# Performance work log

Hardware: AMD Instinct MI355X
Metric: run time of the kernel (lower is better)

Reference implementation:

```python
import jax, jax.numpy as jnp
import numpy as np

N, E = 50000, 800000
IN, HID, H1, H2, OUT = 128, 64, 4, 6, 121
NEG_SLOPE = 0.2


def setup_inputs() -> dict:
    key = jax.random.key(0)
    ks = jax.random.split(key, 16)
    s = 0.1  # weight init scale
    return {
        "x": jax.random.normal(ks[0], (N, IN), jnp.float32),
        "src": jax.random.randint(ks[1], (E,), 0, N),
        "dst": jax.random.randint(ks[2], (E,), 0, N),
        # conv1: in=IN, heads=H1, out=HID, concat
        "W1": jax.random.normal(ks[3], (IN, H1 * HID), jnp.float32) * s,
        "a1_src": jax.random.normal(ks[4], (H1, HID), jnp.float32) * s,
        "a1_dst": jax.random.normal(ks[5], (H1, HID), jnp.float32) * s,
        "b1": jnp.zeros((H1 * HID,), jnp.float32),
        # conv2: in=H1*HID, heads=H1, out=HID, concat, residual
        "W2": jax.random.normal(ks[6], (H1 * HID, H1 * HID), jnp.float32) * s,
        "a2_src": jax.random.normal(ks[7], (H1, HID), jnp.float32) * s,
        "a2_dst": jax.random.normal(ks[8], (H1, HID), jnp.float32) * s,
        "b2": jnp.zeros((H1 * HID,), jnp.float32),
        "Wres2": jax.random.normal(ks[9], (H1 * HID, H1 * HID), jnp.float32) * s,
        # conv3: in=H1*HID, heads=H2, out=OUT, mean (concat=False)
        "W3": jax.random.normal(ks[10], (H1 * HID, H2 * OUT), jnp.float32) * s,
        "a3_src": jax.random.normal(ks[11], (H2, OUT), jnp.float32) * s,
        "a3_dst": jax.random.normal(ks[12], (H2, OUT), jnp.float32) * s,
        "b3": jnp.zeros((OUT,), jnp.float32),
    }


def _segment_softmax(e, seg, n):
    # e: [E, H], softmax over edges sharing the same destination node
    m = jax.ops.segment_max(e, seg, num_segments=n)
    ex = jnp.exp(e - m[seg])
    s = jax.ops.segment_sum(ex, seg, num_segments=n)
    return ex / (s[seg] + 1e-16)


def _gat_conv(x, src, dst, W, a_src, a_dst, b, heads, ch, concat, Wres=None):
    n = x.shape[0]
    h = (x @ W).reshape(n, heads, ch)                       # [N, H, C]
    al_s = jnp.sum(h * a_src, axis=-1)                      # [N, H]
    al_d = jnp.sum(h * a_dst, axis=-1)                      # [N, H]
    e = jax.nn.leaky_relu(al_s[src] + al_d[dst], NEG_SLOPE)  # [E, H]
    alpha = _segment_softmax(e, dst, n)                     # [E, H]
    msg = h[src] * alpha[..., None]                         # [E, H, C]
    out = jax.ops.segment_sum(msg, dst, num_segments=n)     # [N, H, C]
    out = out.reshape(n, heads * ch) if concat else out.mean(axis=1)
    if Wres is not None:
        out = out + x @ Wres
    return out + b


def reference(x, src, dst, W1, a1_src, a1_dst, b1, W2, a2_src, a2_dst, b2,
              Wres2, W3, a3_src, a3_dst, b3):
    n = x.shape[0]
    # PyG GATConv default: add self-loops
    loop = jnp.arange(n, dtype=src.dtype)
    s = jnp.concatenate([src, loop])
    d = jnp.concatenate([dst, loop])
    h = jax.nn.elu(_gat_conv(x, s, d, W1, a1_src, a1_dst, b1, H1, HID, True))
    h = jax.nn.elu(_gat_conv(h, s, d, W2, a2_src, a2_dst, b2, H1, HID, True, Wres=Wres2))
    h = _gat_conv(h, s, d, W3, a3_src, a3_dst, b3, H2, OUT, False)
    return jax.nn.sigmoid(h)
```

## Files before the change

### kernel.cpp

```cpp
#include <hip/hip_runtime.h>
#include <hip/hip_bf16.h>


#define NODES 50000
#define EDGES 800000
#define MPAD  50048
#define C0    25088
#define C1    24912

typedef unsigned short u16;
typedef __attribute__((ext_vector_type(8))) short bf16x8;
typedef __attribute__((ext_vector_type(4))) float f32x4;

__device__ __forceinline__ float bf16f(u16 r) {
    return __uint_as_float(((unsigned)r) << 16);
}
__device__ __forceinline__ u16 f2b(float v) {
    __hip_bfloat16 b = __float2bfloat16(v);
    return *(u16*)&b;
}
__device__ __forceinline__ float blo(unsigned d) { return __uint_as_float(d << 16); }
__device__ __forceinline__ float bhi(unsigned d) { return __uint_as_float(d & 0xffff0000u); }


__global__ void fill_ones_kernel(int* __restrict__ deg, int n) {
    int i = blockIdx.x * blockDim.x + threadIdx.x;
    if (i < n) deg[i] = 1;
}

__global__ void hist_kernel(const int* __restrict__ dst, int* __restrict__ deg, int E) {
    int e = blockIdx.x * blockDim.x + threadIdx.x;
    if (e < E) atomicAdd(&deg[dst[e]], 1);
}

__global__ void deg_bsum_kernel(const int* __restrict__ deg, int* __restrict__ bsum, int n) {
    int tid = threadIdx.x, lane = tid & 63, wid = tid >> 6;
    int i = blockIdx.x * 256 + tid;
    int v = (i < n) ? deg[i] : 0;
    #pragma unroll
    for (int ofs = 32; ofs > 0; ofs >>= 1) v += __shfl_down(v, ofs);
    __shared__ int sp[4];
    if (lane == 0) sp[wid] = v;
    __syncthreads();
    if (tid == 0) bsum[blockIdx.x] = sp[0] + sp[1] + sp[2] + sp[3];
}

__global__ void bsum_scan_kernel(int* __restrict__ bsum, int* __restrict__ row_ptr,
                                 int nb, int n) {
    int tid = threadIdx.x, lane = tid & 63, wid = tid >> 6;
    int v = (tid < nb) ? bsum[tid] : 0;
    int incl = v;
    #pragma unroll
    for (int ofs = 1; ofs < 64; ofs <<= 1) {
        int t = __shfl_up(incl, ofs);
        if (lane >= ofs) incl += t;
    }
    __shared__ int sp[4];
    if (lane == 63) sp[wid] = incl;
    __syncthreads();
    int add = 0;
    for (int k = 0; k < wid; k++) add += sp[k];
    int excl = incl - v + add;
    if (tid < nb) bsum[tid] = excl;
    if (tid == nb - 1) row_ptr[n] = excl + v;
}

__global__ void deg_scan_kernel(const int* __restrict__ deg, const int* __restrict__ bofs,
                                int* __restrict__ row_ptr, int* __restrict__ cursor, int n) {
    int tid = threadIdx.x, lane = tid & 63, wid = tid >> 6;
    int i = blockIdx.x * 256 + tid;
    int v = (i < n) ? deg[i] : 0;
    int incl = v;
    #pragma unroll
    for (int ofs = 1; ofs < 64; ofs <<= 1) {
        int t = __shfl_up(incl, ofs);
        if (lane >= ofs) incl += t;
    }
    __shared__ int sp[4];
    if (lane == 63) sp[wid] = incl;
    __syncthreads();
    int add = bofs[blockIdx.x];
    for (int k = 0; k < wid; k++) add += sp[k];
    int excl = incl - v + add;
    if (i < n) { row_ptr[i] = excl; cursor[i] = excl; }
}

__global__ void scatter_kernel(const int* __restrict__ src, const int* __restrict__ dst,
                               int E, int n, int* __restrict__ cursor, int* __restrict__ csr_src) {
    int e = blockIdx.x * blockDim.x + threadIdx.x;
    if (e < E) {
        int d = dst[e];
        int p = atomicAdd(&cursor[d], 1);
        csr_src[p] = src[e];
    } else if (e < E + n) {
        int i = e - E;
        int p = atomicAdd(&cursor[i], 1);
        csr_src[p] = i;
    }
}


__global__ void prep_weights(
    const float* __restrict__ W1, const float* __restrict__ W2,
    const float* __restrict__ Wres2, const float* __restrict__ W3,
    const float* __restrict__ a1s, const float* __restrict__ a1d,
    const float* __restrict__ a2s, const float* __restrict__ a2d,
    const float* __restrict__ a3s, const float* __restrict__ a3d,
    u16* __restrict__ WT1, u16* __restrict__ WT2, u16* __restrict__ W3sT,
    float* __restrict__ q1t, float* __restrict__ q2t, float* __restrict__ cm) {
    int idx = blockIdx.x * 256 + threadIdx.x;
    if (idx < 32768) {
        int n = idx >> 7, k = idx & 127;
        WT1[idx] = f2b(W1[(size_t)k * 256 + n]);
    } else if ((idx -= 32768) < 131072) {
        int n = idx >> 8, k = idx & 255;
        float v = (n < 256) ? W2[(size_t)k * 256 + n] : Wres2[(size_t)k * 256 + (n - 256)];
        WT2[idx] = f2b(v);
    } else if ((idx -= 131072) < 196608) {
        int n = idx / 1536, q = idx % 1536;
        int h = q >> 8, k = q & 255;
        W3sT[idx] = f2b((n < 121) ? W3[(size_t)k * 726 + h * 121 + n] : 0.f);
    } else if ((idx -= 196608) < 1024) {
        int h = idx >> 7, k = idx & 127;
        int hh = h & 3;
        const float* a = (h < 4) ? a1s : a1d;
        float v = 0.f;
        for (int c = 0; c < 64; c++) v += W1[(size_t)k * 256 + hh * 64 + c] * a[hh * 64 + c];
        q1t[idx] = v;
    } else if ((idx -= 1024) < 2048) {
        int h = idx >> 8, k = idx & 255;
        int hh = h & 3;
        const float* a = (h < 4) ? a2s : a2d;
        float v = 0.f;
        for (int c = 0; c < 64; c++) v += W2[(size_t)k * 256 + hh * 64 + c] * a[hh * 64 + c];
        q2t[idx] = v;
    } else if ((idx -= 2048) < 3072) {
        int o = idx >> 8, k = idx & 255;
        int h = (o < 6) ? o : o - 6;
        const float* a = (o < 6) ? a3s : a3d;
        float v = 0.f;
        for (int c = 0; c < 121; c++) v += W3[(size_t)k * 726 + h * 121 + c] * a[h * 121 + c];
        cm[idx] = v;
    }
}
#define PREP_TOTAL (32768 + 131072 + 196608 + 1024 + 2048 + 3072)


__global__ __launch_bounds__(256) void convx_al1(
    const float* __restrict__ x, const float* __restrict__ q1t,
    u16* __restrict__ A2a, float* __restrict__ alA, int n) {
    int wid = threadIdx.x >> 6, lane = threadIdx.x & 63;
    int i = blockIdx.x * 4 + wid;
    if (i >= n) return;
    float2 xv = *(const float2*)(x + (size_t)i * 128 + lane * 2);
    ushort2 o;
    o.x = f2b(xv.x); o.y = f2b(xv.y);
    *(ushort2*)(A2a + (size_t)i * 128 + lane * 2) = o;
    float p[8];
    #pragma unroll
    for (int h = 0; h < 8; h++) {
        float2 q = *(const float2*)(q1t + h * 128 + lane * 2);
        p[h] = xv.x * q.x + xv.y * q.y;
    }
    #pragma unroll
    for (int ofs = 1; ofs <= 32; ofs <<= 1) {
        #pragma unroll
        for (int h = 0; h < 8; h++) p[h] += __shfl_xor(p[h], ofs);
    }
    if (lane == 0) {
        *(float4*)(alA + (size_t)i * 8)     = make_float4(p[0], p[1], p[2], p[3]);
        *(float4*)(alA + (size_t)i * 8 + 4) = make_float4(p[4], p[5], p[6], p[7]);
    }
}


__global__ __launch_bounds__(256) void gemm_mfma_kernel(
    const u16* __restrict__ A, const u16* __restrict__ B,
    u16* __restrict__ Cb, u16* __restrict__ Cb2,
    int M, int K2, int ldc, int split, int NT, int nrt) {
    __shared__ __align__(16) u16 smem[2][128][40];
    #define As smem[0]
    #define Bs smem[1]
    int b = blockIdx.x;
    int xcd = b & 7, q = b >> 3;
    int ct = q % NT, rb = q / NT;
    int rt = rb * 8 + xcd;
    if (rt >= nrt) return;
    int bm = rt * 128, bn = ct * 128;

    int tid = threadIdx.x;
    int lane = tid & 63;
    int wv = tid >> 6;
    int quad = lane >> 4, lm = lane & 15;
    int wm = (wv & 1) * 64, wn = (wv >> 1) * 64;

    int lrow0 = tid >> 2, lseg0 = (tid & 3) * 8;
    int lrow1 = (tid + 256) >> 2, lseg1 = ((tid + 256) & 3) * 8;
    const u16* Ap0 = A + (size_t)(bm + lrow0) * K2 + lseg0;
    const u16* Ap1 = A + (size_t)(bm + lrow1) * K2 + lseg1;
    const u16* Bp0 = B + (size_t)(bn + lrow0) * K2 + lseg0;
    const u16* Bp1 = B + (size_t)(bn + lrow1) * K2 + lseg1;

    f32x4 zero = {0.f, 0.f, 0.f, 0.f};
    f32x4 acc[4][4];
    #pragma unroll
    for (int i = 0; i < 4; i++)
        #pragma unroll
        for (int j = 0; j < 4; j++) acc[i][j] = zero;

    uint4 pa0 = *(const uint4*)(Ap0), pa1 = *(const uint4*)(Ap1);
    uint4 pb0 = *(const uint4*)(Bp0), pb1 = *(const uint4*)(Bp1);

    for (int k0 = 0; k0 < K2; k0 += 32) {
        *(uint4*)&As[lrow0][lseg0] = pa0;
        *(uint4*)&As[lrow1][lseg1] = pa1;
        *(uint4*)&Bs[lrow0][lseg0] = pb0;
        *(uint4*)&Bs[lrow1][lseg1] = pb1;
        __syncthreads();
        bool more = (k0 + 32) < K2;
        if (more) {
            pa0 = *(const uint4*)(Ap0 + k0 + 32);
            pa1 = *(const uint4*)(Ap1 + k0 + 32);
            pb0 = *(const uint4*)(Bp0 + k0 + 32);
            pb1 = *(const uint4*)(Bp1 + k0 + 32);
        }
        bf16x8 af[4], bfr[4];
        #pragma unroll
        for (int i = 0; i < 4; i++) af[i] = *(const bf16x8*)&As[wm + i * 16 + lm][quad * 8];
        #pragma unroll
        for (int j = 0; j < 4; j++) bfr[j] = *(const bf16x8*)&Bs[wn + j * 16 + lm][quad * 8];
        #pragma unroll
        for (int i = 0; i < 4; i++)
            #pragma unroll
            for (int j = 0; j < 4; j++)
                acc[i][j] = __builtin_amdgcn_mfma_f32_16x16x32_bf16(af[i], bfr[j], acc[i][j], 0, 0, 0);
        __syncthreads();
    }

    u16* Cp = (bn < split) ? (Cb + bn) : (Cb2 + (bn - split));
    u16 (*St)[136] = (u16(*)[136])&smem[0][0][0];
    #pragma unroll
    for (int halfrow = 0; halfrow < 2; ++halfrow) {
        __syncthreads();
        if ((wv & 1) == halfrow) {
            #pragma unroll
            for (int i = 0; i < 4; i++) {
                int lr = i * 16 + quad * 4;
                #pragma unroll
                for (int j = 0; j < 4; j++) {
                    int lc = wn + j * 16 + lm;
                    #pragma unroll
                    for (int r = 0; r < 4; r++)
                        St[lr + r][lc] = f2b(acc[i][j][r]);
                }
            }
        }
        __syncthreads();
        #pragma unroll
        for (int it = 0; it < 4; ++it) {
            int idx = tid + it * 256;
            int row = idx >> 4, seg = idx & 15;
            int grow = bm + halfrow * 64 + row;
            if (grow < M)
                *(uint4*)(Cp + (size_t)grow * ldc + seg * 8) = *(const uint4*)&St[row][seg * 8];
        }
    }
    #undef As
    #undef Bs
}


__global__ __launch_bounds__(256) void gemm_skinny64(
    const u16* __restrict__ A, const u16* __restrict__ B,
    float* __restrict__ C, const float* __restrict__ bias, int count) {
    __shared__ __align__(16) u16 As[64][40];
    __shared__ __align__(16) u16 Bs[128][40];
    int tid = threadIdx.x, lane = tid & 63, wv = tid >> 6;
    int quad = lane >> 4, lm = lane & 15;
    int bm = blockIdx.x * 64;
    int mrow = (wv >> 1) * 32, ncol = (wv & 1) * 64;
    int ar = bm + (tid >> 2);
    if (ar >= count) ar = count - 1;
    const u16* Ap = A + (size_t)ar * 1536 + (tid & 3) * 8;
    int brow0 = tid >> 2, bseg0 = (tid & 3) * 8;
    int brow1 = (tid + 256) >> 2, bseg1 = ((tid + 256) & 3) * 8;
    const u16* Bp0 = B + (size_t)brow0 * 1536 + bseg0;
    const u16* Bp1 = B + (size_t)brow1 * 1536 + bseg1;

    f32x4 zero = {0.f, 0.f, 0.f, 0.f};
    f32x4 acc[2][4];
    #pragma unroll
    for (int i = 0; i < 2; i++)
        #pragma unroll
        for (int j = 0; j < 4; j++) acc[i][j] = zero;

    uint4 pa = *(const uint4*)(Ap);
    uint4 pb0 = *(const uint4*)(Bp0);
    uint4 pb1 = *(const uint4*)(Bp1);

    for (int k0 = 0; k0 < 1536; k0 += 32) {
        *(uint4*)&As[tid >> 2][(tid & 3) * 8] = pa;
        *(uint4*)&Bs[brow0][bseg0] = pb0;
        *(uint4*)&Bs[brow1][bseg1] = pb1;
        __syncthreads();
        bool more = (k0 + 32) < 1536;
        if (more) {
            pa  = *(const uint4*)(Ap + k0 + 32);
            pb0 = *(const uint4*)(Bp0 + k0 + 32);
            pb1 = *(const uint4*)(Bp1 + k0 + 32);
        }
        bf16x8 af[2], bfr[4];
        #pragma unroll
        for (int i = 0; i < 2; i++) af[i] = *(const bf16x8*)&As[mrow + i * 16 + lm][quad * 8];
        #pragma unroll
        for (int j = 0; j < 4; j++) bfr[j] = *(const bf16x8*)&Bs[ncol + j * 16 + lm][quad * 8];
        #pragma unroll
        for (int i = 0; i < 2; i++)
            #pragma unroll
            for (int j = 0; j < 4; j++)
                acc[i][j] = __builtin_amdgcn_mfma_f32_16x16x32_bf16(af[i], bfr[j], acc[i][j], 0, 0, 0);
        __syncthreads();
    }

    #pragma unroll
    for (int i = 0; i < 2; i++) {
        #pragma unroll
        for (int j = 0; j < 4; j++) {
            int col = ncol + j * 16 + lm;
            if (col >= 121) continue;
            int row_base = bm + mrow + i * 16 + quad * 4;
            #pragma unroll
            for (int r = 0; r < 4; r++) {
                int row = row_base + r;
                if (row >= count) continue;
                float v = acc[i][j][r] + bias[col];
                v = 1.f / (1.f + __expf(-v));
                C[(size_t)row * 121 + col] = v;
            }
        }
    }
}


#define ACC8(wt, dv) \
    acc[0] = fmaf(wt, blo(dv.x), acc[0]); acc[1] = fmaf(wt, bhi(dv.x), acc[1]); \
    acc[2] = fmaf(wt, blo(dv.y), acc[2]); acc[3] = fmaf(wt, bhi(dv.y), acc[3]); \
    acc[4] = fmaf(wt, blo(dv.z), acc[4]); acc[5] = fmaf(wt, bhi(dv.z), acc[5]); \
    acc[6] = fmaf(wt, blo(dv.w), acc[6]); acc[7] = fmaf(wt, bhi(dv.w), acc[7]);

template <int NH>
__global__ __launch_bounds__(256) void agg4_fused(
    const u16* __restrict__ f, const float* __restrict__ al8,
    const int* __restrict__ row_ptr, const int* __restrict__ csr_src,
    const float* __restrict__ bias, const u16* __restrict__ resb,
    u16* __restrict__ outb, const float* __restrict__ qpost,
    float* __restrict__ alout, int n) {
    constexpr int NH2 = NH / 2;
    int wid = threadIdx.x >> 6, lane = threadIdx.x & 63;
    int i = blockIdx.x * 4 + wid;
    if (i >= n) return;
    int beg = row_ptr[i], end = row_ptr[i + 1];
    int h_st = lane >> 4;
    int el = lane & 15;
    int half = lane >> 5;
    int c8 = (lane & 31) * 8;
    int wsel = (lane & 24) << 1;
    float ald_st = al8[(size_t)i * 8 + 4 + h_st];
    float acc[8] = {};
    float S = 0.f;
    for (int base = beg; base < end; base += 16) {
        int cnt = min(16, end - base);
        int idxv = csr_src[base + min(el, cnt - 1)];
        float av = al8[(size_t)idxv * 8 + h_st] + ald_st;
        av = av > 0.f ? av : 0.2f * av;
        float ex = __expf(fminf(av, 60.f));
        int e = 0;
        for (; e + 8 <= cnt; e += 8) {
            int s0 = __shfl(idxv, e + half);
            int s1 = __shfl(idxv, e + 2 + half);
            int s2 = __shfl(idxv, e + 4 + half);
            int s3 = __shfl(idxv, e + 6 + half);
            uint4 d0 = *(const uint4*)(f + (size_t)s0 * 256 + c8);
            uint4 d1 = *(const uint4*)(f + (size_t)s1 * 256 + c8);
            uint4 d2 = *(const uint4*)(f + (size_t)s2 * 256 + c8);
            uint4 d3 = *(const uint4*)(f + (size_t)s3 * 256 + c8);
            float w0 = __shfl(ex, wsel | (e + half));
            float w1 = __shfl(ex, wsel | (e + 2 + half));
            float w2 = __shfl(ex, wsel | (e + 4 + half));
            float w3 = __shfl(ex, wsel | (e + 6 + half));
            S += (w0 + w1) + (w2 + w3);
            ACC8(w0, d0);
            ACC8(w1, d1);
            ACC8(w2, d2);
            ACC8(w3, d3);
        }
        for (; e + 4 <= cnt; e += 4) {
            int s0 = __shfl(idxv, e + half);
            int s1 = __shfl(idxv, e + 2 + half);
            uint4 d0 = *(const uint4*)(f + (size_t)s0 * 256 + c8);
            uint4 d1 = *(const uint4*)(f + (size_t)s1 * 256 + c8);
            float w0 = __shfl(ex, wsel | (e + half));
            float w1 = __shfl(ex, wsel | (e + 2 + half));
            S += w0 + w1;
            ACC8(w0, d0);
            ACC8(w1, d1);
        }
        for (; e < cnt; e += 2) {
            int ei = e + half;
            int eu = ei < cnt ? ei : e;
            int s = __shfl(idxv, eu);
            float w = __shfl(ex, wsel | eu);
            if (ei >= cnt) w = 0.f;
            S += w;
            uint4 d = *(const uint4*)(f + (size_t)s * 256 + c8);
            ACC8(w, d);
        }
    }
    #pragma unroll
    for (int k = 0; k < 8; k++) acc[k] += __shfl_xor(acc[k], 32);
    S += __shfl_xor(S, 32);
    float inv = 1.f / (S + 1e-16f);
    float4 b0 = *(const float4*)(bias + c8);
    float4 b1 = *(const float4*)(bias + c8 + 4);
    float v[8];
    v[0] = acc[0] * inv + b0.x; v[1] = acc[1] * inv + b0.y;
    v[2] = acc[2] * inv + b0.z; v[3] = acc[3] * inv + b0.w;
    v[4] = acc[4] * inv + b1.x; v[5] = acc[5] * inv + b1.y;
    v[6] = acc[6] * inv + b1.z; v[7] = acc[7] * inv + b1.w;
    if (resb) {
        uint4 r = *(const uint4*)(resb + (size_t)i * 256 + c8);
        v[0] += blo(r.x); v[1] += bhi(r.x); v[2] += blo(r.y); v[3] += bhi(r.y);
        v[4] += blo(r.z); v[5] += bhi(r.z); v[6] += blo(r.w); v[7] += bhi(r.w);
    }
    #pragma unroll
    for (int k = 0; k < 8; k++) v[k] = v[k] > 0.f ? v[k] : (__expf(v[k]) - 1.f);
    uint4 o;
    o.x = (unsigned)f2b(v[0]) | ((unsigned)f2b(v[1]) << 16);
    o.y = (unsigned)f2b(v[2]) | ((unsigned)f2b(v[3]) << 16);
    o.z = (unsigned)f2b(v[4]) | ((unsigned)f2b(v[5]) << 16);
    o.w = (unsigned)f2b(v[6]) | ((unsigned)f2b(v[7]) << 16);
    if (half == 0)
        *(uint4*)(outb + (size_t)i * 256 + c8) = o;
    if (NH > 0) {
        float rv[8];
        rv[0] = blo(o.x); rv[1] = bhi(o.x); rv[2] = blo(o.y); rv[3] = bhi(o.y);
        rv[4] = blo(o.z); rv[5] = bhi(o.z); rv[6] = blo(o.w); rv[7] = bhi(o.w);
        int hbase = half * NH2;
        float p[NH2 > 0 ? NH2 : 1];
        #pragma unroll
        for (int h = 0; h < NH2; h++) {
            const float* qp = qpost + (size_t)(hbase + h) * 256 + c8;
            float4 qa = *(const float4*)(qp);
            float4 qb = *(const float4*)(qp + 4);
            p[h] = rv[0] * qa.x + rv[1] * qa.y + rv[2] * qa.z + rv[3] * qa.w
                 + rv[4] * qb.x + rv[5] * qb.y + rv[6] * qb.z + rv[7] * qb.w;
        }
        #pragma unroll
        for (int ofs = 1; ofs <= 16; ofs <<= 1) {
            #pragma unroll
            for (int h = 0; h < NH2; h++) p[h] += __shfl_xor(p[h], ofs);
        }
        if ((lane & 31) == 0) {
            float* ap = alout + (size_t)i * NH + hbase;
            if (NH2 == 4) {
                *(float4*)ap = make_float4(p[0], p[1], p[2], p[3]);
            } else if (NH2 == 6) {
                if (half == 0) {
                    *(float4*)ap = make_float4(p[0], p[1], p[2], p[3]);
                    *(float2*)(ap + 4) = make_float2(p[4], p[5]);
                } else {
                    *(float2*)ap = make_float2(p[0], p[1]);
                    *(float4*)(ap + 2) = make_float4(p[2], p[3], p[4], p[5]);
                }
            } else {
                #pragma unroll
                for (int h = 0; h < NH2; h++) ap[h] = p[h];
            }
        }
    }
}


__global__ __launch_bounds__(256) void aggS_fused(
    const u16* __restrict__ x, const float* __restrict__ al3,
    const int* __restrict__ row_ptr, const int* __restrict__ csr_src,
    u16* __restrict__ S, int node0, int count) {
    __shared__ int s_i[4][16];
    __shared__ float s_w[4][96];
    __shared__ float s_sum[4][6];
    int wid = threadIdx.x >> 6, lane = threadIdx.x & 63;
    int li = blockIdx.x * 4 + wid;
    if (li >= count) return;
    int i = node0 + li;
    int beg = row_ptr[i], end = row_ptr[i + 1];
    int c4 = lane * 4;
    int e16 = lane & 15;
    int hA = lane >> 4;
    int hB = 4 + (lane >> 4);
    float aldA = al3[(size_t)i * 12 + 6 + hA];
    float aldB = (lane < 32) ? al3[(size_t)i * 12 + 6 + hB] : 0.f;
    float acc[6][4] = {};
    if (lane < 6) s_sum[wid][lane] = 0.f;
    for (int base = beg; base < end; base += 16) {
        int cnt = min(16, end - base);
        int idxe = csr_src[base + min(e16, cnt - 1)];
        if (lane < 16) s_i[wid][lane] = idxe;
        float vA = al3[(size_t)idxe * 12 + hA] + aldA;
        vA = vA > 0.f ? vA : 0.2f * vA;
        float exA = __expf(fminf(vA, 60.f));
        if (e16 < cnt) s_w[wid][e16 * 6 + hA] = exA;
        float exB = 0.f;
        if (lane < 32) {
            float vB = al3[(size_t)idxe * 12 + hB] + aldB;
            vB = vB > 0.f ? vB : 0.2f * vB;
            exB = __expf(fminf(vB, 60.f));
            if (e16 < cnt) s_w[wid][e16 * 6 + hB] = exB;
        }
        float sA = (e16 < cnt) ? exA : 0.f;
        sA += __shfl_xor(sA, 1); sA += __shfl_xor(sA, 2);
        sA += __shfl_xor(sA, 4); sA += __shfl_xor(sA, 8);
        float sB = (lane < 32 && e16 < cnt) ? exB : 0.f;
        sB += __shfl_xor(sB, 1); sB += __shfl_xor(sB, 2);
        sB += __shfl_xor(sB, 4); sB += __shfl_xor(sB, 8);
        if (e16 == 0) {
            s_sum[wid][hA] += sA;
            if (lane < 32) s_sum[wid][hB] += sB;
        }
        int e = 0;
        for (; e + 4 <= cnt; e += 4) {
            int s0 = s_i[wid][e],     s1 = s_i[wid][e + 1];
            int s2 = s_i[wid][e + 2], s3 = s_i[wid][e + 3];
            uint2 d0 = *(const uint2*)(x + (size_t)s0 * 256 + c4);
            uint2 d1 = *(const uint2*)(x + (size_t)s1 * 256 + c4);
            uint2 d2 = *(const uint2*)(x + (size_t)s2 * 256 + c4);
            uint2 d3 = *(const uint2*)(x + (size_t)s3 * 256 + c4);
            float f00 = blo(d0.x), f01 = bhi(d0.x), f02 = blo(d0.y), f03 = bhi(d0.y);
            float f10 = blo(d1.x), f11 = bhi(d1.x), f12 = blo(d1.y), f13 = bhi(d1.y);
            float f20 = blo(d2.x), f21 = bhi(d2.x), f22 = blo(d2.y), f23 = bhi(d2.y);
            float f30 = blo(d3.x), f31 = bhi(d3.x), f32 = blo(d3.y), f33 = bhi(d3.y);
            #pragma unroll
            for (int hh = 0; hh < 6; hh++) {
                float w0 = s_w[wid][e * 6 + hh];
                float w1 = s_w[wid][(e + 1) * 6 + hh];
                float w2 = s_w[wid][(e + 2) * 6 + hh];
                float w3 = s_w[wid][(e + 3) * 6 + hh];
                acc[hh][0] = fmaf(w0, f00, acc[hh][0]);
                acc[hh][1] = fmaf(w0, f01, acc[hh][1]);
                acc[hh][2] = fmaf(w0, f02, acc[hh][2]);
                acc[hh][3] = fmaf(w0, f03, acc[hh][3]);
                acc[hh][0] = fmaf(w1, f10, acc[hh][0]);
                acc[hh][1] = fmaf(w1, f11, acc[hh][1]);
                acc[hh][2] = fmaf(w1, f12, acc[hh][2]);
                acc[hh][3] = fmaf(w1, f13, acc[hh][3]);
                acc[hh][0] = fmaf(w2, f20, acc[hh][0]);
                acc[hh][1] = fmaf(w2, f21, acc[hh][1]);
                acc[hh][2] = fmaf(w2, f22, acc[hh][2]);
                acc[hh][3] = fmaf(w2, f23, acc[hh][3]);
                acc[hh][0] = fmaf(w3, f30, acc[hh][0]);
                acc[hh][1] = fmaf(w3, f31, acc[hh][1]);
                acc[hh][2] = fmaf(w3, f32, acc[hh][2]);
                acc[hh][3] = fmaf(w3, f33, acc[hh][3]);
            }
        }
        for (; e < cnt; e++) {
            int s = s_i[wid][e];
            uint2 d = *(const uint2*)(x + (size_t)s * 256 + c4);
            float v0 = blo(d.x), v1 = bhi(d.x), v2 = blo(d.y), v3 = bhi(d.y);
            #pragma unroll
            for (int hh = 0; hh < 6; hh++) {
                float w = s_w[wid][e * 6 + hh];
                acc[hh][0] = fmaf(w, v0, acc[hh][0]);
                acc[hh][1] = fmaf(w, v1, acc[hh][1]);
                acc[hh][2] = fmaf(w, v2, acc[hh][2]);
                acc[hh][3] = fmaf(w, v3, acc[hh][3]);
            }
        }
    }
    #pragma unroll
    for (int hh = 0; hh < 6; hh++) {
        float inv = 1.f / (6.f * (s_sum[wid][hh] + 1e-16f));
        ushort4 o;
        o.x = f2b(acc[hh][0] * inv);
        o.y = f2b(acc[hh][1] * inv);
        o.z = f2b(acc[hh][2] * inv);
        o.w = f2b(acc[hh][3] * inv);
        *(ushort4*)(S + (size_t)li * 1536 + hh * 256 + c4) = o;
    }
}


extern "C" void kernel_launch(void* const* d_in, const int* in_sizes, int n_in,
                              void* d_out, int out_size, void* d_ws, size_t ws_size,
                              hipStream_t stream) {
    const float* x      = (const float*)d_in[0];
    const int*   src    = (const int*)d_in[1];
    const int*   dst    = (const int*)d_in[2];
    const float* W1     = (const float*)d_in[3];
    const float* a1_src = (const float*)d_in[4];
    const float* a1_dst = (const float*)d_in[5];
    const float* b1     = (const float*)d_in[6];
    const float* W2     = (const float*)d_in[7];
    const float* a2_src = (const float*)d_in[8];
    const float* a2_dst = (const float*)d_in[9];
    const float* b2     = (const float*)d_in[10];
    const float* Wres2  = (const float*)d_in[11];
    const float* W3     = (const float*)d_in[12];
    const float* a3_src = (const float*)d_in[13];
    const float* a3_dst = (const float*)d_in[14];
    const float* b3     = (const float*)d_in[15];
    float* out = (float*)d_out;

    const int N = NODES, E = EDGES;
    const int EN = E + N;
    const int NB = (N + 255) / 256;
    const int NRT = MPAD / 128;

    char* p = (char*)d_ws;
    auto alloc = [&](size_t bytes) -> char* {
        char* r = p;
        p += (bytes + 511) & ~(size_t)511;
        return r;
    };
    int*   row_ptr = (int*)alloc((size_t)(N + 1) * sizeof(int));
    int*   cursor  = (int*)alloc((size_t)N * sizeof(int));
    int*   deg     = (int*)alloc((size_t)N * sizeof(int));
    int*   bsum    = (int*)alloc(256 * sizeof(int));
    int*   csr_src = (int*)alloc((size_t)EN * sizeof(int));
    float* alA     = (float*)alloc((size_t)N * 8 * sizeof(float));
    float* alB     = (float*)alloc((size_t)N * 8 * sizeof(float));
    float* al3     = (float*)alloc((size_t)N * 12 * sizeof(float));
    float* q1t     = (float*)alloc((size_t)8 * 128 * sizeof(float));
    float* q2t     = (float*)alloc((size_t)8 * 256 * sizeof(float));
    float* cm      = (float*)alloc((size_t)12 * 256 * sizeof(float));
    u16*   WT1     = (u16*)alloc((size_t)256 * 128 * sizeof(u16));
    u16*   WT2     = (u16*)alloc((size_t)512 * 256 * sizeof(u16));
    u16*   W3sT    = (u16*)alloc((size_t)128 * 1536 * sizeof(u16));
    u16*   o2b     = (u16*)alloc((size_t)MPAD * 256 * sizeof(u16));
    const size_t A2B_B  = (size_t)MPAD * 256 * sizeof(u16);
    const size_t F1B_B  = (size_t)N * 256 * sizeof(u16);
    const size_t RESB_B = (size_t)N * 256 * sizeof(u16);
    const size_t S_B    = (size_t)C0 * 1536 * sizeof(u16);
    size_t r2_bytes = A2B_B + F1B_B + RESB_B;
    if (S_B > r2_bytes) r2_bytes = S_B;
    char* r2 = alloc(r2_bytes + 1024);
    u16* A2b  = (u16*)r2;
    u16* f1b  = (u16*)(r2 + A2B_B);
    u16* resb = (u16*)(r2 + A2B_B + F1B_B);
    u16* A2a  = (u16*)(r2 + A2B_B + F1B_B);
    u16* Sb   = (u16*)r2;
    (void)ws_size; (void)n_in; (void)in_sizes; (void)out_size;

    fill_ones_kernel<<<NB, 256, 0, stream>>>(deg, N);
    hist_kernel<<<(E + 255) / 256, 256, 0, stream>>>(dst, deg, E);
    deg_bsum_kernel<<<NB, 256, 0, stream>>>(deg, bsum, N);
    bsum_scan_kernel<<<1, 256, 0, stream>>>(bsum, row_ptr, NB, N);
    deg_scan_kernel<<<NB, 256, 0, stream>>>(deg, bsum, row_ptr, cursor, N);
    scatter_kernel<<<(E + N + 255) / 256, 256, 0, stream>>>(src, dst, E, N, cursor, csr_src);

    int nwb = (N + 3) / 4;

    prep_weights<<<(PREP_TOTAL + 255) / 256, 256, 0, stream>>>(
        W1, W2, Wres2, W3, a1_src, a1_dst, a2_src, a2_dst, a3_src, a3_dst,
        WT1, WT2, W3sT, q1t, q2t, cm);

    convx_al1<<<nwb, 256, 0, stream>>>(x, q1t, A2a, alA, N);
    {
        int nblk = 8 * ((NRT + 7) / 8) * 2;
        gemm_mfma_kernel<<<nblk, 256, 0, stream>>>(A2a, WT1, f1b, nullptr,
                                                   N, 128, 256, 9999, 2, NRT);
    }
    agg4_fused<8><<<nwb, 256, 0, stream>>>(f1b, alA, row_ptr, csr_src, b1, nullptr,
                                           A2b, q2t, alB, N);

    {
        int nblk = 8 * ((NRT + 7) / 8) * 4;
        gemm_mfma_kernel<<<nblk, 256, 0, stream>>>(A2b, WT2, f1b, resb,
                                                   N, 256, 256, 256, 4, NRT);
    }
    agg4_fused<12><<<nwb, 256, 0, stream>>>(f1b, alB, row_ptr, csr_src, b2, resb,
                                            o2b, cm, al3, N);

    {
        aggS_fused<<<(C0 + 3) / 4, 256, 0, stream>>>(o2b, al3, row_ptr, csr_src, Sb, 0, C0);
        gemm_skinny64<<<(C0 + 63) / 64, 256, 0, stream>>>(Sb, W3sT, out, b3, C0);
        aggS_fused<<<(C1 + 3) / 4, 256, 0, stream>>>(o2b, al3, row_ptr, csr_src, Sb, C0, C1);
        gemm_skinny64<<<(C1 + 63) / 64, 256, 0, stream>>>(Sb, W3sT, out + (size_t)C0 * 121, b3, C1);
    }
}
```

Before: 597.9 us.

## Load full-K tiles into LDS once and template GEMM on K and tile count

Replaces the K-stepped double-register-prefetch GEMM with a version that loads the entire K extent of the A and B tiles into shared memory up front, then runs a fully unrolled MFMA loop with no per-step barriers. K and the column-tile count become template parameters. This removes per-iteration syncs and global-to-LDS staging stalls, but raises LDS use (about 68KB for K=256), which may cut occupancy and leaves no overlap between load and compute.

```diff
diff --git a/kernel.cpp b/kernel.cpp
--- a/kernel.cpp
+++ b/kernel.cpp
@@ -174,13 +174,14 @@
 }
 
 
-__global__ __launch_bounds__(256) void gemm_mfma_kernel(
+template <int K2, int NT>
+__global__ __launch_bounds__(256) void gemm_fullk(
     const u16* __restrict__ A, const u16* __restrict__ B,
     u16* __restrict__ Cb, u16* __restrict__ Cb2,
-    int M, int K2, int ldc, int split, int NT, int nrt) {
-    __shared__ __align__(16) u16 smem[2][128][40];
-    #define As smem[0]
-    #define Bs smem[1]
+    int M, int ldc, int split, int nrt) {
+    constexpr int KP = K2 + 8;
+    __shared__ __align__(16) u16 As[128][KP];
+    __shared__ __align__(16) u16 Bs[128][KP];
     int b = blockIdx.x;
     int xcd = b & 7, q = b >> 3;
     int ct = q % NT, rb = q / NT;
@@ -189,17 +190,20 @@
     int bm = rt * 128, bn = ct * 128;
 
     int tid = threadIdx.x;
-    int lane = tid & 63;
-    int wv = tid >> 6;
+    int lane = tid & 63, wv = tid >> 6;
     int quad = lane >> 4, lm = lane & 15;
     int wm = (wv & 1) * 64, wn = (wv >> 1) * 64;
 
-    int lrow0 = tid >> 2, lseg0 = (tid & 3) * 8;
-    int lrow1 = (tid + 256) >> 2, lseg1 = ((tid + 256) & 3) * 8;
-    const u16* Ap0 = A + (size_t)(bm + lrow0) * K2 + lseg0;
-    const u16* Ap1 = A + (size_t)(bm + lrow1) * K2 + lseg1;
-    const u16* Bp0 = B + (size_t)(bn + lrow0) * K2 + lseg0;
-    const u16* Bp1 = B + (size_t)(bn + lrow1) * K2 + lseg1;
+    constexpr int SEGROW = K2 / 8;
+    constexpr int ITER = 128 * SEGROW / 256;
+    #pragma unroll
+    for (int it = 0; it < ITER; ++it) {
+        int s = tid + it * 256;
+        int row = s / SEGROW, c8 = (s % SEGROW) * 8;
+        *(uint4*)&As[row][c8] = *(const uint4*)(A + (size_t)(bm + row) * K2 + c8);
+        *(uint4*)&Bs[row][c8] = *(const uint4*)(B + (size_t)(bn + row) * K2 + c8);
+    }
+    __syncthreads();
 
     f32x4 zero = {0.f, 0.f, 0.f, 0.f};
     f32x4 acc[4][4];
@@ -208,37 +212,22 @@
         #pragma unroll
         for (int j = 0; j < 4; j++) acc[i][j] = zero;
 
-    uint4 pa0 = *(const uint4*)(Ap0), pa1 = *(const uint4*)(Ap1);
-    uint4 pb0 = *(const uint4*)(Bp0), pb1 = *(const uint4*)(Bp1);
-
+    #pragma unroll
     for (int k0 = 0; k0 < K2; k0 += 32) {
-        *(uint4*)&As[lrow0][lseg0] = pa0;
-        *(uint4*)&As[lrow1][lseg1] = pa1;
-        *(uint4*)&Bs[lrow0][lseg0] = pb0;
-        *(uint4*)&Bs[lrow1][lseg1] = pb1;
-        __syncthreads();
-        bool more = (k0 + 32) < K2;
-        if (more) {
-            pa0 = *(const uint4*)(Ap0 + k0 + 32);
-            pa1 = *(const uint4*)(Ap1 + k0 + 32);
-            pb0 = *(const uint4*)(Bp0 + k0 + 32);
-            pb1 = *(const uint4*)(Bp1 + k0 + 32);
-        }
         bf16x8 af[4], bfr[4];
         #pragma unroll
-        for (int i = 0; i < 4; i++) af[i] = *(const bf16x8*)&As[wm + i * 16 + lm][quad * 8];
-        #pragma unroll
-        for (int j = 0; j < 4; j++) bfr[j] = *(const bf16x8*)&Bs[wn + j * 16 + lm][quad * 8];
+        for (int i = 0; i < 4; i++) af[i] = *(const bf16x8*)&As[wm + i * 16 + lm][k0 + quad * 8];
+        #pragma unroll
+        for (int j = 0; j < 4; j++) bfr[j] = *(const bf16x8*)&Bs[wn + j * 16 + lm][k0 + quad * 8];
         #pragma unroll
         for (int i = 0; i < 4; i++)
             #pragma unroll
             for (int j = 0; j < 4; j++)
                 acc[i][j] = __builtin_amdgcn_mfma_f32_16x16x32_bf16(af[i], bfr[j], acc[i][j], 0, 0, 0);
-        __syncthreads();
     }
 
     u16* Cp = (bn < split) ? (Cb + bn) : (Cb2 + (bn - split));
-    u16 (*St)[136] = (u16(*)[136])&smem[0][0][0];
+    u16 (*St)[136] = (u16(*)[136])&As[0][0];
     #pragma unroll
     for (int halfrow = 0; halfrow < 2; ++halfrow) {
         __syncthreads();
@@ -265,8 +254,6 @@
                 *(uint4*)(Cp + (size_t)grow * ldc + seg * 8) = *(const uint4*)&St[row][seg * 8];
         }
     }
-    #undef As
-    #undef Bs
 }
 
 
@@ -666,16 +653,16 @@
     convx_al1<<<nwb, 256, 0, stream>>>(x, q1t, A2a, alA, N);
     {
         int nblk = 8 * ((NRT + 7) / 8) * 2;
-        gemm_mfma_kernel<<<nblk, 256, 0, stream>>>(A2a, WT1, f1b, nullptr,
-                                                   N, 128, 256, 9999, 2, NRT);
+        gemm_fullk<128, 2><<<nblk, 256, 0, stream>>>(A2a, WT1, f1b, nullptr,
+                                                     N, 256, 9999, NRT);
     }
     agg4_fused<8><<<nwb, 256, 0, stream>>>(f1b, alA, row_ptr, csr_src, b1, nullptr,
                                            A2b, q2t, alB, N);
 
     {
         int nblk = 8 * ((NRT + 7) / 8) * 4;
-        gemm_mfma_kernel<<<nblk, 256, 0, stream>>>(A2b, WT2, f1b, resb,
-                                                   N, 256, 256, 256, 4, NRT);
+        gemm_fullk<256, 4><<<nblk, 256, 0, stream>>>(A2b, WT2, f1b, resb,
+                                                     N, 256, 256, NRT);
     }
     agg4_fused<12><<<nwb, 256, 0, stream>>>(f1b, alB, row_ptr, csr_src, b2, resb,
                                             o2b, cm, al3, N);
```

Result: no change. 609.2 us (+1.9%).
